# Optimization experiments

Measured on AMD Instinct MI355X. Metric: run time of the kernel, lower is better.

## Reference

```python
import jax, jax.numpy as jnp
import numpy as np

VOCAB = 32000
EMBED = 128
HIDDEN = 2048
LAYERS = 3
BATCH = 16


def setup_inputs() -> dict:
    key = jax.random.key(0)
    ks = jax.random.split(key, 4 + 4 * LAYERS)
    inp = {}
    inp["tokens"] = jax.random.randint(ks[0], (1, BATCH), 0, VOCAB, dtype=jnp.int64)
    inp["hidden"] = jax.random.normal(ks[1], (LAYERS, BATCH, HIDDEN), dtype=jnp.float32)
    s_e = 1.0 / np.sqrt(EMBED)
    s_h = 1.0 / np.sqrt(HIDDEN)
    inp["emb"] = jax.random.normal(ks[2], (VOCAB, EMBED), dtype=jnp.float32) * s_e
    for l in range(LAYERS):
        in_dim = EMBED if l == 0 else HIDDEN
        k0, k1, k2, k3 = jax.random.split(ks[4 + l], 4)
        inp[f"W_ih{l}"] = jax.random.normal(k0, (3 * HIDDEN, in_dim), dtype=jnp.float32) * s_h
        inp[f"W_hh{l}"] = jax.random.normal(k1, (3 * HIDDEN, HIDDEN), dtype=jnp.float32) * s_h
        inp[f"b_ih{l}"] = jax.random.normal(k2, (3 * HIDDEN,), dtype=jnp.float32) * s_h
        inp[f"b_hh{l}"] = jax.random.normal(k3, (3 * HIDDEN,), dtype=jnp.float32) * s_h
    inp["W_out"] = jax.random.normal(ks[3], (VOCAB, HIDDEN), dtype=jnp.float32) * s_h
    inp["b_out"] = jnp.zeros((VOCAB,), dtype=jnp.float32)
    return inp


def _gru_cell(x, h, W_ih, W_hh, b_ih, b_hh):
    # PyTorch GRU gate math; x: (B, in), h: (B, H)
    gi = x @ W_ih.T + b_ih  # (B, 3H)
    gh = h @ W_hh.T + b_hh  # (B, 3H)
    i_r, i_z, i_n = jnp.split(gi, 3, axis=-1)
    h_r, h_z, h_n = jnp.split(gh, 3, axis=-1)
    r = jax.nn.sigmoid(i_r + h_r)
    z = jax.nn.sigmoid(i_z + h_z)
    n = jnp.tanh(i_n + r * h_n)
    return (1.0 - z) * n + z * h


def reference(tokens, hidden, emb,
              W_ih0, W_hh0, b_ih0, b_hh0,
              W_ih1, W_hh1, b_ih1, b_hh1,
              W_ih2, W_hh2, b_ih2, b_hh2,
              W_out, b_out):
    # embedding + ReLU; tokens: (1, B) -> x: (B, E) (seq_len = 1)
    x = jax.nn.relu(emb[tokens[0]])
    Ws = [(W_ih0, W_hh0, b_ih0, b_hh0),
          (W_ih1, W_hh1, b_ih1, b_hh1),
          (W_ih2, W_hh2, b_ih2, b_hh2)]
    new_h = []
    inp = x
    for l, (Wih, Whh, bih, bhh) in enumerate(Ws):
        h_l = _gru_cell(inp, hidden[l], Wih, Whh, bih, bhh)
        new_h.append(h_l)
        inp = h_l  # top-layer output feeds next layer
    new_hidden = jnp.stack(new_h, axis=0)  # (L, B, H)
    logits = inp @ W_out.T + b_out  # (B, V)
    logp = jax.nn.log_softmax(logits, axis=1)
    return logp, new_hidden
```

## Files before the change

kernel.cpp:

```cpp
#include <hip/hip_runtime.h>
#include <cmath>


#define BB 16
#define HH 2048
#define EE 128
#define VV 32000
#define G3H (3 * HH)

__device__ __forceinline__ void fma4(float& a, const float4 w, const float4 x) {
  a = fmaf(w.x, x.x, a); a = fmaf(w.y, x.y, a);
  a = fmaf(w.z, x.z, a); a = fmaf(w.w, x.w, a);
}

__device__ __forceinline__ float foldpair(float a, float b, int m, int lane) {
  float t = (lane & m) ? a : b;
  t = __shfl_xor(t, m, 64);
  return ((lane & m) ? b : a) + t;
}

__device__ __forceinline__ float sel16(const float a[16], int i) {
  float s0 = (i & 1) ? a[1]  : a[0];
  float s1 = (i & 1) ? a[3]  : a[2];
  float s2 = (i & 1) ? a[5]  : a[4];
  float s3 = (i & 1) ? a[7]  : a[6];
  float s4 = (i & 1) ? a[9]  : a[8];
  float s5 = (i & 1) ? a[11] : a[10];
  float s6 = (i & 1) ? a[13] : a[12];
  float s7 = (i & 1) ? a[15] : a[14];
  float t0 = (i & 2) ? s1 : s0;
  float t1 = (i & 2) ? s3 : s2;
  float t2 = (i & 2) ? s5 : s4;
  float t3 = (i & 2) ? s7 : s6;
  float u0 = (i & 4) ? t1 : t0;
  float u1 = (i & 4) ? t3 : t2;
  return (i & 8) ? u1 : u0;
}

template<bool BIAS>
__device__ __forceinline__
void gemv8r4b(const float* __restrict__ x, const float* __restrict__ W,
              const float* __restrict__ bias, float* __restrict__ dst,
              int ldd, int row0, int bgrp, int lane)
{
  float acc[32];
  #pragma unroll
  for (int i = 0; i < 32; ++i) acc[i] = 0.f;

  const int kb = lane * 4;
  const float* xb = x + (size_t)bgrp * 4 * HH + kb;
  const float* Wr = W + (size_t)row0 * HH + kb;

  #pragma unroll 1
  for (int it = 0; it < 8; ++it) {
    const int k = it * 256;
    float4 wv[8];
    #pragma unroll
    for (int r = 0; r < 8; ++r)
      wv[r] = *(const float4*)(Wr + (size_t)r * HH + k);
    float4 xv[4];
    #pragma unroll
    for (int b = 0; b < 4; ++b)
      xv[b] = *(const float4*)(xb + b * HH + k);
    #pragma unroll
    for (int r = 0; r < 8; ++r)
      #pragma unroll
      for (int b = 0; b < 4; ++b) fma4(acc[r * 4 + b], wv[r], xv[b]);
  }

  #pragma unroll
  for (int j = 0; j < 16; ++j) acc[j] = foldpair(acc[j], acc[j + 16], 1, lane);
  #pragma unroll
  for (int j = 0; j < 8; ++j)  acc[j] = foldpair(acc[j], acc[j + 8], 2, lane);
  #pragma unroll
  for (int j = 0; j < 4; ++j)  acc[j] = foldpair(acc[j], acc[j + 4], 4, lane);
  #pragma unroll
  for (int j = 0; j < 2; ++j)  acc[j] = foldpair(acc[j], acc[j + 2], 8, lane);
  acc[0] = foldpair(acc[0], acc[1], 16, lane);
  acc[0] += __shfl_xor(acc[0], 32, 64);

  const int idx = ((lane & 1) << 4) | ((lane & 2) << 2) | (lane & 4)
                | ((lane & 8) >> 2) | ((lane & 16) >> 4);
  const int r = idx >> 2;
  const int b = idx & 3;
  if (lane < 32) {
    float o = acc[0];
    if (BIAS) o += bias[row0 + r];
    dst[(size_t)(bgrp * 4 + b) * ldd + row0 + r] = o;
  }
}

__global__ __launch_bounds__(256, 2)
void gru_l0(const float* __restrict__ emb, const int* __restrict__ tokens,
            const float* __restrict__ hprev,
            const float* __restrict__ Wih0, const float* __restrict__ Whh0,
            float* __restrict__ gi, float* __restrict__ gh)
{
  const int tid  = threadIdx.x;
  const int lane = tid & 63;
  const int wv   = tid >> 6;
  const int bx   = blockIdx.x;

  if (bx < 128) {
    const int kk = lane & 15;
    const int rg = lane >> 4;
    const int u  = bx * 4 + wv;
    const int row0 = u * 12 + rg * 3;
    float acc[3][16];
    #pragma unroll
    for (int r = 0; r < 3; ++r)
      #pragma unroll
      for (int b = 0; b < 16; ++b) acc[r][b] = 0.f;

    #pragma unroll
    for (int it = 0; it < 2; ++it) {
      const int k = it * 64 + kk * 4;
      const float4 w0 = *(const float4*)(Wih0 + (size_t)row0 * EE + k);
      const float4 w1 = *(const float4*)(Wih0 + (size_t)(row0 + 1) * EE + k);
      const float4 w2 = *(const float4*)(Wih0 + (size_t)(row0 + 2) * EE + k);
      #pragma unroll
      for (int b = 0; b < 16; ++b) {
        float4 xv = *(const float4*)(emb + (size_t)tokens[b] * EE + k);
        xv.x = fmaxf(xv.x, 0.f); xv.y = fmaxf(xv.y, 0.f);
        xv.z = fmaxf(xv.z, 0.f); xv.w = fmaxf(xv.w, 0.f);
        fma4(acc[0][b], w0, xv);
        fma4(acc[1][b], w1, xv);
        fma4(acc[2][b], w2, xv);
      }
    }
    #pragma unroll
    for (int r = 0; r < 3; ++r) {
      #pragma unroll
      for (int b = 0; b < 16; ++b) {
        float a = acc[r][b];
        a += __shfl_xor(a, 1, 64);
        a += __shfl_xor(a, 2, 64);
        a += __shfl_xor(a, 4, 64);
        a += __shfl_xor(a, 8, 64);
        acc[r][b] = a;
      }
    }
    #pragma unroll
    for (int r = 0; r < 3; ++r)
      gi[(size_t)kk * G3H + row0 + r] = sel16(acc[r], kk);
  } else {
    const int u = bx - 128;
    gemv8r4b<false>(hprev, Whh0, nullptr, gh, G3H, u * 8, wv, lane);
  }
}

__global__ __launch_bounds__(256, 2)
void gru_l12(const float* __restrict__ xprev, const float* __restrict__ hl,
             const float* __restrict__ Wih, const float* __restrict__ Whh,
             float* __restrict__ gi, float* __restrict__ gh)
{
  const int lane = threadIdx.x & 63;
  const int wv   = threadIdx.x >> 6;
  const int bx   = blockIdx.x;
  if (bx < 768) gemv8r4b<false>(xprev, Wih, nullptr, gi, G3H, bx * 8, wv, lane);
  else          gemv8r4b<false>(hl, Whh, nullptr, gh, G3H, (bx - 768) * 8, wv, lane);
}

__global__ __launch_bounds__(256)
void gru_epi(const float* __restrict__ gi, const float* __restrict__ gh,
             const float* __restrict__ bih, const float* __restrict__ bhh,
             const float* __restrict__ hprev, float* __restrict__ hout)
{
  const int idx = blockIdx.x * 256 + threadIdx.x;
  const int j = idx & (HH - 1);
  const size_t base = (size_t)(idx >> 11) * G3H;
  const float ir  = gi[base + j]          + bih[j];
  const float iz  = gi[base + HH + j]     + bih[HH + j];
  const float in_ = gi[base + 2 * HH + j] + bih[2 * HH + j];
  const float hr  = gh[base + j]          + bhh[j];
  const float hz  = gh[base + HH + j]     + bhh[HH + j];
  const float hn  = gh[base + 2 * HH + j] + bhh[2 * HH + j];
  const float r = 1.f / (1.f + expf(-(ir + hr)));
  const float z = 1.f / (1.f + expf(-(iz + hz)));
  const float n = tanhf(in_ + r * hn);
  hout[idx] = (1.f - z) * n + z * hprev[idx];
}

__global__ __launch_bounds__(256, 2)
void out_kernel(const float* __restrict__ h2, const float* __restrict__ Wout,
                const float* __restrict__ bout, float* __restrict__ logits)
{
  const int lane = threadIdx.x & 63;
  const int wv   = threadIdx.x >> 6;
  gemv8r4b<true>(h2, Wout, bout, logits, VV, blockIdx.x * 8, wv, lane);
}

__global__ __launch_bounds__(1024)
void lsm_kernel(float* __restrict__ logp)
{
  const int b   = blockIdx.x;
  const int tid = threadIdx.x;
  float* row = logp + (size_t)b * VV;
  const float4* r4 = (const float4*)row;
  __shared__ float red[16];
  const int wv = tid >> 6, ln = tid & 63;

  float m = -3.4e38f;
  for (int i = tid; i < VV / 4; i += 1024) {
    float4 v = r4[i];
    m = fmaxf(m, fmaxf(fmaxf(v.x, v.y), fmaxf(v.z, v.w)));
  }
  #pragma unroll
  for (int s = 1; s < 64; s <<= 1) m = fmaxf(m, __shfl_xor(m, s, 64));
  if (ln == 0) red[wv] = m;
  __syncthreads();
  if (tid == 0) {
    float mm = red[0];
    for (int w = 1; w < 16; ++w) mm = fmaxf(mm, red[w]);
    red[0] = mm;
  }
  __syncthreads();
  const float M = red[0];
  __syncthreads();

  float s = 0.f;
  for (int i = tid; i < VV / 4; i += 1024) {
    float4 v = r4[i];
    s += expf(v.x - M) + expf(v.y - M) + expf(v.z - M) + expf(v.w - M);
  }
  #pragma unroll
  for (int t = 1; t < 64; t <<= 1) s += __shfl_xor(s, t, 64);
  if (ln == 0) red[wv] = s;
  __syncthreads();
  if (tid == 0) {
    float ss = 0.f;
    for (int w = 0; w < 16; ++w) ss += red[w];
    red[0] = M + logf(ss);
  }
  __syncthreads();
  const float L = red[0];

  float4* w4 = (float4*)row;
  for (int i = tid; i < VV / 4; i += 1024) {
    float4 v = r4[i];
    v.x -= L; v.y -= L; v.z -= L; v.w -= L;
    w4[i] = v;
  }
}

extern "C" void kernel_launch(void* const* d_in, const int* in_sizes, int n_in,
                              void* d_out, int out_size, void* d_ws, size_t ws_size,
                              hipStream_t stream)
{
  const int*   tokens = (const int*)d_in[0];
  const float* hidden = (const float*)d_in[1];
  const float* emb    = (const float*)d_in[2];
  const float* Wih0 = (const float*)d_in[3];
  const float* Whh0 = (const float*)d_in[4];
  const float* bih0 = (const float*)d_in[5];
  const float* bhh0 = (const float*)d_in[6];
  const float* Wih1 = (const float*)d_in[7];
  const float* Whh1 = (const float*)d_in[8];
  const float* bih1 = (const float*)d_in[9];
  const float* bhh1 = (const float*)d_in[10];
  const float* Wih2 = (const float*)d_in[11];
  const float* Whh2 = (const float*)d_in[12];
  const float* bih2 = (const float*)d_in[13];
  const float* bhh2 = (const float*)d_in[14];
  const float* Wout = (const float*)d_in[15];
  const float* bout = (const float*)d_in[16];

  float* outp = (float*)d_out;
  float* logp = outp;
  float* hnew = outp + (size_t)BB * VV;
  float* h0 = hnew;
  float* h1 = hnew + BB * HH;
  float* h2 = hnew + 2 * BB * HH;

  float* gi = (float*)d_ws;
  float* gh = gi + (size_t)BB * G3H;

  gru_l0<<<896, 256, 0, stream>>>(emb, tokens, hidden, Wih0, Whh0, gi, gh);
  gru_epi<<<128, 256, 0, stream>>>(gi, gh, bih0, bhh0, hidden, h0);
  gru_l12<<<1536, 256, 0, stream>>>(h0, hidden + BB * HH, Wih1, Whh1, gi, gh);
  gru_epi<<<128, 256, 0, stream>>>(gi, gh, bih1, bhh1, hidden + BB * HH, h1);
  gru_l12<<<1536, 256, 0, stream>>>(h1, hidden + 2 * BB * HH, Wih2, Whh2, gi, gh);
  gru_epi<<<128, 256, 0, stream>>>(gi, gh, bih2, bhh2, hidden + 2 * BB * HH, h2);
  out_kernel<<<4000, 256, 0, stream>>>(h2, Wout, bout, logp);
  lsm_kernel<<<16, 1024, 0, stream>>>(logp);
}
```

Before: 217.0 us.

## Split-K GEMVs with all-batch register x, LDS-staged weight streaming and partial planes

Replaces the per-block 8-row, 4-batch GEMV with a split-K scheme. Each wave holds all 16 batch vectors for one 256-wide K slice in registers and streams many weight rows through LDS using global_load_lds. Partial sums go to 8 K-slice planes, which the GRU epilogue and the log-softmax kernel then reduce, with the output bias folded into log-softmax. The aim is to load the weights once instead of once per group of 4 batches. The cost is extra partial-plane traffic and a full vmcnt wait per 8-row chunk, which leaves little overlap between loading and computing.

```diff
diff --git a/kernel.cpp b/kernel.cpp
--- a/kernel.cpp
+++ b/kernel.cpp
@@ -11,6 +11,12 @@
 __device__ __forceinline__ void fma4(float& a, const float4 w, const float4 x) {
   a = fmaf(w.x, x.x, a); a = fmaf(w.y, x.y, a);
   a = fmaf(w.z, x.z, a); a = fmaf(w.w, x.w, a);
+}
+
+__device__ __forceinline__ void glds16(const float* g, float* l) {
+  __builtin_amdgcn_global_load_lds(
+      (__attribute__((address_space(1))) void*)(g),
+      (__attribute__((address_space(3))) void*)(l), 16, 0, 0);
 }
 
 __device__ __forceinline__ float foldpair(float a, float b, int m, int lane) {
@@ -37,65 +43,66 @@
   return (i & 8) ? u1 : u0;
 }
 
-template<bool BIAS>
 __device__ __forceinline__
-void gemv8r4b(const float* __restrict__ x, const float* __restrict__ W,
-              const float* __restrict__ bias, float* __restrict__ dst,
-              int ldd, int row0, int bgrp, int lane)
-{
-  float acc[32];
+void gemv_stream(const float* __restrict__ x,
+                 const float* __restrict__ W,
+                 float* __restrict__ planes,
+                 int R, int slice, int row0, int nrows,
+                 int lane, float* lds)
+{
+  const int ko = slice * 256 + lane * 4;
+  float4 xv[16];
   #pragma unroll
-  for (int i = 0; i < 32; ++i) acc[i] = 0.f;
-
-  const int kb = lane * 4;
-  const float* xb = x + (size_t)bgrp * 4 * HH + kb;
-  const float* Wr = W + (size_t)row0 * HH + kb;
-
-  #pragma unroll 1
-  for (int it = 0; it < 8; ++it) {
-    const int k = it * 256;
-    float4 wv[8];
-    #pragma unroll
-    for (int r = 0; r < 8; ++r)
-      wv[r] = *(const float4*)(Wr + (size_t)r * HH + k);
-    float4 xv[4];
-    #pragma unroll
-    for (int b = 0; b < 4; ++b)
-      xv[b] = *(const float4*)(xb + b * HH + k);
-    #pragma unroll
-    for (int r = 0; r < 8; ++r)
-      #pragma unroll
-      for (int b = 0; b < 4; ++b) fma4(acc[r * 4 + b], wv[r], xv[b]);
-  }
-
-  #pragma unroll
-  for (int j = 0; j < 16; ++j) acc[j] = foldpair(acc[j], acc[j + 16], 1, lane);
-  #pragma unroll
-  for (int j = 0; j < 8; ++j)  acc[j] = foldpair(acc[j], acc[j + 8], 2, lane);
-  #pragma unroll
-  for (int j = 0; j < 4; ++j)  acc[j] = foldpair(acc[j], acc[j + 4], 4, lane);
-  #pragma unroll
-  for (int j = 0; j < 2; ++j)  acc[j] = foldpair(acc[j], acc[j + 2], 8, lane);
-  acc[0] = foldpair(acc[0], acc[1], 16, lane);
-  acc[0] += __shfl_xor(acc[0], 32, 64);
+  for (int b = 0; b < 16; ++b)
+    xv[b] = *(const float4*)(x + b * HH + ko);
 
   const int idx = ((lane & 1) << 4) | ((lane & 2) << 2) | (lane & 4)
                 | ((lane & 8) >> 2) | ((lane & 16) >> 4);
-  const int r = idx >> 2;
-  const int b = idx & 3;
-  if (lane < 32) {
-    float o = acc[0];
-    if (BIAS) o += bias[row0 + r];
-    dst[(size_t)(bgrp * 4 + b) * ldd + row0 + r] = o;
-  }
-}
-
-__global__ __launch_bounds__(256, 2)
+  const int rr = idx >> 4;
+  const int bb = idx & 15;
+
+  for (int m = 0; m < nrows; m += 8) {
+    #pragma unroll
+    for (int r = 0; r < 8; ++r)
+      glds16(W + (size_t)(row0 + m + r) * HH + ko, lds + r * 256);
+    asm volatile("s_waitcnt vmcnt(0)" ::: "memory");
+    __builtin_amdgcn_sched_barrier(0);
+
+    #pragma unroll
+    for (int g = 0; g < 4; ++g) {
+      float acc[32];
+      #pragma unroll
+      for (int i = 0; i < 32; ++i) acc[i] = 0.f;
+      const float4 w0 = *(const float4*)(lds + (g * 2 + 0) * 256 + lane * 4);
+      const float4 w1 = *(const float4*)(lds + (g * 2 + 1) * 256 + lane * 4);
+      #pragma unroll
+      for (int b = 0; b < 16; ++b) {
+        fma4(acc[b],      w0, xv[b]);
+        fma4(acc[16 + b], w1, xv[b]);
+      }
+      #pragma unroll
+      for (int j = 0; j < 16; ++j) acc[j] = foldpair(acc[j], acc[j + 16], 1, lane);
+      #pragma unroll
+      for (int j = 0; j < 8; ++j)  acc[j] = foldpair(acc[j], acc[j + 8], 2, lane);
+      #pragma unroll
+      for (int j = 0; j < 4; ++j)  acc[j] = foldpair(acc[j], acc[j + 4], 4, lane);
+      #pragma unroll
+      for (int j = 0; j < 2; ++j)  acc[j] = foldpair(acc[j], acc[j + 2], 8, lane);
+      acc[0] = foldpair(acc[0], acc[1], 16, lane);
+      acc[0] += __shfl_xor(acc[0], 32, 64);
+      if (lane < 32)
+        planes[(size_t)(slice * 16 + bb) * R + row0 + m + g * 2 + rr] = acc[0];
+    }
+  }
+}
+
+__global__ __launch_bounds__(256, 3)
 void gru_l0(const float* __restrict__ emb, const int* __restrict__ tokens,
             const float* __restrict__ hprev,
             const float* __restrict__ Wih0, const float* __restrict__ Whh0,
-            float* __restrict__ gi, float* __restrict__ gh)
-{
+            float* __restrict__ gi_flat, float* __restrict__ ghP)
+{
+  __shared__ float lds[4 * 2048];
   const int tid  = threadIdx.x;
   const int lane = tid & 63;
   const int wv   = tid >> 6;
@@ -142,68 +149,109 @@
     }
     #pragma unroll
     for (int r = 0; r < 3; ++r)
-      gi[(size_t)kk * G3H + row0 + r] = sel16(acc[r], kk);
+      gi_flat[(size_t)kk * G3H + row0 + r] = sel16(acc[r], kk);
   } else {
-    const int u = bx - 128;
-    gemv8r4b<false>(hprev, Whh0, nullptr, gh, G3H, u * 8, wv, lane);
-  }
-}
-
-__global__ __launch_bounds__(256, 2)
+    const int w = (bx - 128) * 4 + wv;
+    gemv_stream(hprev, Whh0, ghP, G3H, w >> 7, (w & 127) * 48, 48,
+                lane, lds + wv * 2048);
+  }
+}
+
+__global__ __launch_bounds__(256, 3)
 void gru_l12(const float* __restrict__ xprev, const float* __restrict__ hl,
              const float* __restrict__ Wih, const float* __restrict__ Whh,
-             float* __restrict__ gi, float* __restrict__ gh)
-{
+             float* __restrict__ giP, float* __restrict__ ghP)
+{
+  __shared__ float lds[4 * 2048];
   const int lane = threadIdx.x & 63;
   const int wv   = threadIdx.x >> 6;
   const int bx   = blockIdx.x;
-  if (bx < 768) gemv8r4b<false>(xprev, Wih, nullptr, gi, G3H, bx * 8, wv, lane);
-  else          gemv8r4b<false>(hl, Whh, nullptr, gh, G3H, (bx - 768) * 8, wv, lane);
-}
-
+  if (bx < 256) {
+    const int w = bx * 4 + wv;
+    gemv_stream(xprev, Wih, giP, G3H, w >> 7, (w & 127) * 48, 48,
+                lane, lds + wv * 2048);
+  } else {
+    const int w = (bx - 256) * 4 + wv;
+    gemv_stream(hl, Whh, ghP, G3H, w >> 7, (w & 127) * 48, 48,
+                lane, lds + wv * 2048);
+  }
+}
+
+template<bool GI8>
 __global__ __launch_bounds__(256)
-void gru_epi(const float* __restrict__ gi, const float* __restrict__ gh,
+void gru_epi(const float* __restrict__ gi_flat, const float* __restrict__ giP,
+             const float* __restrict__ ghP,
              const float* __restrict__ bih, const float* __restrict__ bhh,
              const float* __restrict__ hprev, float* __restrict__ hout)
 {
   const int idx = blockIdx.x * 256 + threadIdx.x;
   const int j = idx & (HH - 1);
-  const size_t base = (size_t)(idx >> 11) * G3H;
-  const float ir  = gi[base + j]          + bih[j];
-  const float iz  = gi[base + HH + j]     + bih[HH + j];
-  const float in_ = gi[base + 2 * HH + j] + bih[2 * HH + j];
-  const float hr  = gh[base + j]          + bhh[j];
-  const float hz  = gh[base + HH + j]     + bhh[HH + j];
-  const float hn  = gh[base + 2 * HH + j] + bhh[2 * HH + j];
+  const int b = idx >> 11;
+  float ir, iz, in_;
+  if (GI8) {
+    ir = 0.f; iz = 0.f; in_ = 0.f;
+    #pragma unroll
+    for (int s = 0; s < 8; ++s) {
+      const size_t base = (size_t)(s * 16 + b) * G3H;
+      ir  += giP[base + j];
+      iz  += giP[base + HH + j];
+      in_ += giP[base + 2 * HH + j];
+    }
+  } else {
+    const size_t base = (size_t)b * G3H;
+    ir  = gi_flat[base + j];
+    iz  = gi_flat[base + HH + j];
+    in_ = gi_flat[base + 2 * HH + j];
+  }
+  float hr = 0.f, hz = 0.f, hn = 0.f;
+  #pragma unroll
+  for (int s = 0; s < 8; ++s) {
+    const size_t base = (size_t)(s * 16 + b) * G3H;
+    hr += ghP[base + j];
+    hz += ghP[base + HH + j];
+    hn += ghP[base + 2 * HH + j];
+  }
+  ir += bih[j]; iz += bih[HH + j]; in_ += bih[2 * HH + j];
+  hr += bhh[j]; hz += bhh[HH + j]; hn += bhh[2 * HH + j];
   const float r = 1.f / (1.f + expf(-(ir + hr)));
   const float z = 1.f / (1.f + expf(-(iz + hz)));
   const float n = tanhf(in_ + r * hn);
   hout[idx] = (1.f - z) * n + z * hprev[idx];
 }
 
-__global__ __launch_bounds__(256, 2)
+__global__ __launch_bounds__(256, 3)
 void out_kernel(const float* __restrict__ h2, const float* __restrict__ Wout,
-                const float* __restrict__ bout, float* __restrict__ logits)
-{
+                float* __restrict__ opP)
+{
+  __shared__ float lds[4 * 2048];
   const int lane = threadIdx.x & 63;
   const int wv   = threadIdx.x >> 6;
-  gemv8r4b<true>(h2, Wout, bout, logits, VV, blockIdx.x * 8, wv, lane);
+  const int w = blockIdx.x * 4 + wv;
+  const int slice = w / 250;
+  const int part  = w % 250;
+  gemv_stream(h2, Wout, opP, VV, slice, part * 128, 128, lane, lds + wv * 2048);
 }
 
 __global__ __launch_bounds__(1024)
-void lsm_kernel(float* __restrict__ logp)
+void lsm_kernel(const float* __restrict__ opP, const float* __restrict__ bout,
+                float* __restrict__ logp)
 {
   const int b   = blockIdx.x;
   const int tid = threadIdx.x;
   float* row = logp + (size_t)b * VV;
-  const float4* r4 = (const float4*)row;
   __shared__ float red[16];
   const int wv = tid >> 6, ln = tid & 63;
 
   float m = -3.4e38f;
   for (int i = tid; i < VV / 4; i += 1024) {
-    float4 v = r4[i];
-    m = fmaxf(m, fmaxf(fmaxf(v.x, v.y), fmaxf(v.z, v.w)));
+    float4 a = ((const float4*)bout)[i];
+    #pragma unroll
+    for (int s = 0; s < 8; ++s) {
+      const float4 p = ((const float4*)(opP + (size_t)(s * 16 + b) * VV))[i];
+      a.x += p.x; a.y += p.y; a.z += p.z; a.w += p.w;
+    }
+    ((float4*)row)[i] = a;
+    m = fmaxf(m, fmaxf(fmaxf(a.x, a.y), fmaxf(a.z, a.w)));
   }
   #pragma unroll
   for (int s = 1; s < 64; s <<= 1) m = fmaxf(m, __shfl_xor(m, s, 64));
@@ -220,7 +268,7 @@
 
   float s = 0.f;
   for (int i = tid; i < VV / 4; i += 1024) {
-    float4 v = r4[i];
+    float4 v = ((const float4*)row)[i];
     s += expf(v.x - M) + expf(v.y - M) + expf(v.z - M) + expf(v.w - M);
   }
   #pragma unroll
@@ -235,11 +283,10 @@
   __syncthreads();
   const float L = red[0];
 
-  float4* w4 = (float4*)row;
   for (int i = tid; i < VV / 4; i += 1024) {
-    float4 v = r4[i];
+    float4 v = ((const float4*)row)[i];
     v.x -= L; v.y -= L; v.z -= L; v.w -= L;
-    w4[i] = v;
+    ((float4*)row)[i] = v;
   }
 }
 
@@ -272,15 +319,17 @@
   float* h1 = hnew + BB * HH;
   float* h2 = hnew + 2 * BB * HH;
 
-  float* gi = (float*)d_ws;
-  float* gh = gi + (size_t)BB * G3H;
-
-  gru_l0<<<896, 256, 0, stream>>>(emb, tokens, hidden, Wih0, Whh0, gi, gh);
-  gru_epi<<<128, 256, 0, stream>>>(gi, gh, bih0, bhh0, hidden, h0);
-  gru_l12<<<1536, 256, 0, stream>>>(h0, hidden + BB * HH, Wih1, Whh1, gi, gh);
-  gru_epi<<<128, 256, 0, stream>>>(gi, gh, bih1, bhh1, hidden + BB * HH, h1);
-  gru_l12<<<1536, 256, 0, stream>>>(h1, hidden + 2 * BB * HH, Wih2, Whh2, gi, gh);
-  gru_epi<<<128, 256, 0, stream>>>(gi, gh, bih2, bhh2, hidden + 2 * BB * HH, h2);
-  out_kernel<<<4000, 256, 0, stream>>>(h2, Wout, bout, logp);
-  lsm_kernel<<<16, 1024, 0, stream>>>(logp);
-}
+  float* gi_flat = (float*)d_ws;
+  float* giP = gi_flat + (size_t)BB * G3H;
+  float* ghP = giP + (size_t)8 * BB * G3H;
+  float* opP = ghP + (size_t)8 * BB * G3H;
+
+  gru_l0<<<384, 256, 0, stream>>>(emb, tokens, hidden, Wih0, Whh0, gi_flat, ghP);
+  gru_epi<false><<<128, 256, 0, stream>>>(gi_flat, nullptr, ghP, bih0, bhh0, hidden, h0);
+  gru_l12<<<512, 256, 0, stream>>>(h0, hidden + BB * HH, Wih1, Whh1, giP, ghP);
+  gru_epi<true><<<128, 256, 0, stream>>>(nullptr, giP, ghP, bih1, bhh1, hidden + BB * HH, h1);
+  gru_l12<<<512, 256, 0, stream>>>(h1, hidden + 2 * BB * HH, Wih2, Whh2, giP, ghP);
+  gru_epi<true><<<128, 256, 0, stream>>>(nullptr, giP, ghP, bih2, bhh2, hidden + 2 * BB * HH, h2);
+  out_kernel<<<500, 256, 0, stream>>>(h2, Wout, opP);
+  lsm_kernel<<<16, 1024, 0, stream>>>(opP, bout, logp);
+}
```

Result: slower. 231.2 us (+6.5%).
